# Optimization experiments

Measured on AMD Instinct MI355X. Metric: run time of the kernel, lower is better.

The kernel has to match this reference:

```python
import jax, jax.numpy as jnp
import numpy as np
from jax import lax

BATCH = 512
NUM_ITER = 5
NUM_CLASSES = 10
NUM_PRIMARY = 32 * 6 * 6  # 1152
CAPS_IN = 8
CAPS_OUT = 16
EPS = 1e-5


def _bn(x, g, b):
    # training-mode batchnorm over (N,H,W) per channel, NCHW
    m = x.mean(axis=(0, 2, 3), keepdims=True)
    v = x.var(axis=(0, 2, 3), keepdims=True)
    return g[None, :, None, None] * (x - m) * lax.rsqrt(v + EPS) + b[None, :, None, None]


def _conv(x, w, b, stride):
    y = lax.conv_general_dilated(x, w, (stride, stride), 'VALID',
                                 dimension_numbers=('NCHW', 'OIHW', 'NCHW'))
    return y + b[None, :, None, None]


def _squash(s):
    # per source: n / (n^2 + 1) * x
    n = jnp.linalg.norm(s, axis=-1, keepdims=True)
    return n / (n * n + 1.0) * s


def setup_inputs() -> dict:
    key = jax.random.key(0)
    ks = jax.random.split(key, 10)
    d = {
        'x': jax.random.normal(ks[0], (BATCH, 1, 28, 28), jnp.float32),
        'conv1_w': jax.random.normal(ks[1], (256, 1, 9, 9), jnp.float32) * 0.05,
        'conv1_b': jnp.zeros((256,), jnp.float32),
        'bn1_g': jnp.ones((256,), jnp.float32),
        'bn1_b': jnp.zeros((256,), jnp.float32),
        # 8 branch convs of (32,256,9,9) stacked into one (256,256,9,9) conv
        'conv2_w': jax.random.normal(ks[2], (256, 256, 9, 9), jnp.float32) * 0.01,
        'conv2_b': jnp.zeros((256,), jnp.float32),
        'bn2_g': jnp.ones((256,), jnp.float32),
        'bn2_b': jnp.zeros((256,), jnp.float32),
        'W': jax.random.normal(ks[3], (NUM_CLASSES, NUM_PRIMARY, CAPS_IN, CAPS_OUT), jnp.float32),
    }
    return d


def reference(x, conv1_w, conv1_b, bn1_g, bn1_b, conv2_w, conv2_b, bn2_g, bn2_b, W):
    B = x.shape[0]
    # input conv: (B,1,28,28) -> (B,256,20,20)
    y = jax.nn.relu(_bn(_conv(x, conv1_w, conv1_b, 1), bn1_g, bn1_b))
    # primary caps conv (8 branches fused): (B,256,6,6)
    z = jax.nn.relu(_bn(_conv(y, conv2_w, conv2_b, 2), bn2_g, bn2_b))
    # capsules: (B,8,32,6,6) -> (B, 1152, 8); capsule dim = branch index
    u = z.reshape(B, CAPS_IN, NUM_PRIMARY).transpose(0, 2, 1)
    # prediction vectors u_hat: (B, 10, 1152, 16)
    u_hat = jnp.einsum('bid,jide->bjie', u, W)

    def routing_step(b_log, _):
        c = jax.nn.softmax(b_log, axis=1)              # over 10 output caps
        s = jnp.einsum('bji,bjie->bje', c, u_hat)      # (B,10,16)
        v = _squash(s)
        b_log = b_log + jnp.einsum('bjie,bje->bji', u_hat, v)
        return b_log, v

    b0 = jnp.zeros((B, NUM_CLASSES, NUM_PRIMARY), u_hat.dtype)
    _, vs = lax.scan(routing_step, b0, None, length=NUM_ITER)
    return vs[-1]  # (B, 10, 16)
```

## Files before the change

### kernel.cpp

```cpp
#include <hip/hip_runtime.h>

typedef unsigned short u16;
typedef unsigned int   u32;
typedef __attribute__((ext_vector_type(8))) short bf16x8;
typedef __attribute__((ext_vector_type(4))) float f32x4;

__device__ __forceinline__ float bf2f(u16 u) { return __uint_as_float(((u32)u) << 16); }
__device__ __forceinline__ float bflo(u32 u) { return __uint_as_float(u << 16); }
__device__ __forceinline__ float bfhi(u32 u) { return __uint_as_float(u & 0xffff0000u); }
__device__ __forceinline__ u16 f2bf(float f) {
    u32 x = __float_as_uint(f);
    x += 0x7fffu + ((x >> 16) & 1u);
    return (u16)(x >> 16);
}
__device__ __forceinline__ u16 f2h(float f) {
    _Float16 h = (_Float16)f;
    return __builtin_bit_cast(u16, h);
}
__device__ __forceinline__ float h2f(u16 u) {
    return (float)__builtin_bit_cast(_Float16, u);
}

__global__ __launch_bounds__(256) void repack_w2_kernel(const float* __restrict__ w2,
                                                        u16* __restrict__ w2r) {
    int idx = blockIdx.x * 256 + threadIdx.x;
    int cil = idx & 31;
    int co  = (idx >> 5) & 255;
    int ccc = (idx >> 13) & 7;
    int kk  = idx >> 16;
    int ci  = ccc * 32 + cil;
    w2r[idx] = f2bf(w2[(size_t)co * 20736 + (size_t)ci * 81 + kk]);
}

__global__ __launch_bounds__(256) void repack_W_kernel(const float* __restrict__ W,
                                                       float* __restrict__ Wt2) {
    int idx = blockIdx.x * 256 + threadIdx.x;
    int d  = idx & 7;
    int je = (idx >> 3) % 160;
    int i  = idx / 1280;
    int j = je >> 4, e = je & 15;
    Wt2[idx] = W[(((size_t)j * 1152 + i) * 8 + d) * 16 + e];
}

__global__ __launch_bounds__(256) void conv1_kernel(const float* __restrict__ x,
                                                    const float* __restrict__ w1,
                                                    const float* __restrict__ b1,
                                                    u16* __restrict__ y,
                                                    float* __restrict__ sum1,
                                                    float* __restrict__ sumsq1) {
    __shared__ float xs[784];
    const int b = blockIdx.x;
    const int t = threadIdx.x;
    const float* xb = x + (size_t)b * 784;
    for (int idx = t; idx < 784; idx += 256) xs[idx] = xb[idx];
    float w[81];
#pragma unroll
    for (int q = 0; q < 81; ++q) w[q] = w1[(size_t)t * 81 + q];
    const float bias = b1[t];
    __syncthreads();

    float sl = 0.f, ssl = 0.f;
    u16* yb = y + (size_t)b * 400 * 256 + t;
    for (int oh = 0; oh < 20; ++oh) {
        float acc[20];
#pragma unroll
        for (int ow = 0; ow < 20; ++ow) acc[ow] = bias;
#pragma unroll
        for (int kh = 0; kh < 9; ++kh) {
            const float4* rp = (const float4*)(&xs[(oh + kh) * 28]);
            float r[28];
#pragma unroll
            for (int k4 = 0; k4 < 7; ++k4) {
                float4 f = rp[k4];
                r[k4 * 4 + 0] = f.x; r[k4 * 4 + 1] = f.y;
                r[k4 * 4 + 2] = f.z; r[k4 * 4 + 3] = f.w;
            }
#pragma unroll
            for (int kw = 0; kw < 9; ++kw) {
                const float wv = w[kh * 9 + kw];
#pragma unroll
                for (int ow = 0; ow < 20; ++ow)
                    acc[ow] = fmaf(wv, r[ow + kw], acc[ow]);
            }
        }
#pragma unroll
        for (int ow = 0; ow < 20; ++ow) {
            u16 q = f2bf(acc[ow]);
            float rv = bf2f(q);
            sl += rv; ssl += rv * rv;
            yb[(size_t)(oh * 20 + ow) * 256] = q;
        }
    }
    atomicAdd(&sum1[t], sl);
    atomicAdd(&sumsq1[t], ssl);
}

__global__ void finalize_bn_kernel(const float* __restrict__ sum,
                                   const float* __restrict__ sumsq,
                                   const float* __restrict__ gam,
                                   const float* __restrict__ bet,
                                   float* __restrict__ scale,
                                   float* __restrict__ shift, float inv_n) {
    int c = threadIdx.x;
    float m = sum[c] * inv_n;
    float var = sumsq[c] * inv_n - m * m;
    float sc = gam[c] * rsqrtf(var + 1e-5f);
    scale[c] = sc;
    shift[c] = bet[c] - m * sc;
}

__global__ __launch_bounds__(256) void bnpack_kernel(u32* __restrict__ y32,
                                                     const float* __restrict__ scale1,
                                                     const float* __restrict__ shift1) {
    const int b = blockIdx.x;
    const int t = threadIdx.x;
    const int c2 = (t & 127) * 2;
    const float s0 = scale1[c2],     s1 = scale1[c2 + 1];
    const float h0 = shift1[c2],     h1 = shift1[c2 + 1];
    u32* base = y32 + (size_t)b * 51200;
    for (int q = 0; q < 200; ++q) {
        const int idx = t + q * 256;
        u32 v = base[idx];
        float a = fmaxf(0.f, fmaf(s0, bflo(v), h0));
        float c = fmaxf(0.f, fmaf(s1, bfhi(v), h1));
        base[idx] = (u32)f2bf(a) | ((u32)f2bf(c) << 16);
    }
}

__global__ __launch_bounds__(256, 2) void conv2_mfma_kernel(const u16* __restrict__ y,
                                                            const u16* __restrict__ w2r,
                                                            const float* __restrict__ b2,
                                                            float* __restrict__ z_raw,
                                                            float* __restrict__ sum2,
                                                            float* __restrict__ sumsq2) {
    __shared__ __align__(16) u16 stg[240 * 136];
    const int g  = blockIdx.x >> 1;
    const int cb = (blockIdx.x & 1) * 128;
    const int b0 = g * 2;
    const int t = threadIdx.x;
    const int wave = t >> 6, lane = t & 63;
    const int n16 = lane & 15, quad = lane >> 4;
    const int img = wave & 1, c64 = wave >> 1;

    f32x4 zero = {0.f, 0.f, 0.f, 0.f};
    f32x4 acc[4][3];
#pragma unroll
    for (int ct = 0; ct < 4; ++ct)
#pragma unroll
        for (int pt = 0; pt < 3; ++pt) acc[ct][pt] = zero;

    int brow[3];
#pragma unroll
    for (int pt = 0; pt < 3; ++pt) {
        int pos = pt * 16 + n16; if (pos > 35) pos = 35;
        const int oh = (pos * 43) >> 8;
        const int ow = pos - oh * 6;
        brow[pt] = (img * 6 + oh) * 20 + 2 * ow;
    }

    const int laneoff = (cb + c64 * 64 + n16) * 32 + quad * 8;

    bf16x8 abuf[3][4];
    bf16x8 bbuf[2][3];

    auto loadA = [&](bf16x8 (&dst)[4], const u16* basep, int ittv) {
        const u16* wa = basep + (ittv >> 2) * 65536 + (ittv & 3) * 8192;
#pragma unroll
        for (int ct = 0; ct < 4; ++ct)
            dst[ct] = *((const bf16x8*)(wa + ct * 512));
    };
    auto loadB = [&](bf16x8 (&dst)[3], int ittv) {
        const int kw = ittv >> 2, ccc = ittv & 3;
#pragma unroll
        for (int pt = 0; pt < 3; ++pt)
            dst[pt] = *((const bf16x8*)(stg + (brow[pt] + kw) * 136
                                        + ccc * 32 + quad * 8));
    };

    {
        const u16* w0 = w2r + laneoff;
        loadA(abuf[0], w0, 0);
        loadA(abuf[1], w0, 1);
        loadA(abuf[2], w0, 2);
    }

    for (int kh = 0; kh < 9; ++kh) {
        for (int cp = 0; cp < 2; ++cp) {
            __syncthreads();
#pragma unroll
            for (int q = 0; q < 15; ++q) {
                const int v = t + q * 256;
                const int rI = v >> 4, c16 = v & 15;
                const int i2 = (rI >= 120) ? 1 : 0;
                const int rr = rI - i2 * 120;
                const int oh = rr / 20;
                const int iw = rr - oh * 20;
                const int ip = (2 * oh + kh) * 20 + iw;
                const uint4 d = *((const uint4*)(y + ((size_t)(b0 + i2) * 400 + ip) * 256
                                                 + cp * 128 + c16 * 8));
                *((uint4*)(stg + rI * 136 + c16 * 8)) = d;
            }
            __syncthreads();

            const int khn = (cp == 1) ? kh + 1 : kh;
            const int cpn = cp ^ 1;
            const u16* wbase = w2r + (size_t)kh * 589824 + (size_t)cp * 32768 + laneoff;
            const u16* wnext = w2r + (size_t)khn * 589824 + (size_t)cpn * 32768 + laneoff;

            loadB(bbuf[0], 0);
            loadB(bbuf[1], 1);

#pragma unroll
            for (int itt = 0; itt < 36; ++itt) {
                const int a_i = itt % 3, b_i = itt % 2;
#pragma unroll
                for (int ct = 0; ct < 4; ++ct)
#pragma unroll
                    for (int pt = 0; pt < 3; ++pt)
                        acc[ct][pt] = __builtin_amdgcn_mfma_f32_16x16x32_bf16(
                            abuf[a_i][ct], bbuf[b_i][pt], acc[ct][pt], 0, 0, 0);
                if (itt < 33) loadA(abuf[a_i], wbase, itt + 3);
                else          loadA(abuf[a_i], wnext, itt + 3 - 36);
                if (itt < 34) loadB(bbuf[b_i], itt + 2);
            }
        }
    }

#pragma unroll
    for (int ct = 0; ct < 4; ++ct) {
#pragma unroll
        for (int r = 0; r < 4; ++r) {
            const int co = cb + c64 * 64 + ct * 16 + quad * 4 + r;
            const float bias = b2[co];
            float s = 0.f, ss = 0.f;
#pragma unroll
            for (int pt = 0; pt < 3; ++pt) {
                const int pos = pt * 16 + n16;
                if (pos < 36) {
                    float v = acc[ct][pt][r] + bias;
                    z_raw[((size_t)(b0 + img) * 256 + co) * 36 + pos] = v;
                    s += v; ss += v * v;
                }
            }
#pragma unroll
            for (int m = 1; m < 16; m <<= 1) {
                s  += __shfl_xor(s,  m, 64);
                ss += __shfl_xor(ss, m, 64);
            }
            if (n16 == 0) { atomicAdd(&sum2[co], s); atomicAdd(&sumsq2[co], ss); }
        }
    }
}

__global__ __launch_bounds__(256) void ubuild_kernel(const float* __restrict__ z_raw,
                                                     const float* __restrict__ scale2,
                                                     const float* __restrict__ shift2,
                                                     u16* __restrict__ ut16) {
    const int b = blockIdx.x;
    const int t = threadIdx.x;
    const int d = t >> 5, m = t & 31;
    const float sc = scale2[t], sh = shift2[t];
    const float* zp = z_raw + ((size_t)b * 256 + t) * 36;
    u32* up = (u32*)(ut16 + ((size_t)b * 8 + d) * 1152 + m * 36);
#pragma unroll
    for (int q = 0; q < 18; ++q) {
        float v0 = fmaxf(0.f, fmaf(sc, zp[2 * q],     sh));
        float v1 = fmaxf(0.f, fmaf(sc, zp[2 * q + 1], sh));
        up[q] = (u32)f2h(v0) | ((u32)f2h(v1) << 16);
    }
}

__global__ __launch_bounds__(256) void uhat_kernel(const u16* __restrict__ ut16,
                                                   const float* __restrict__ Wt2,
                                                   u16* __restrict__ u_hat,
                                                   float* __restrict__ s0g) {
    __shared__ float utl[8 * 8 * 144];
    const int bg = blockIdx.x >> 3;
    const int ic = blockIdx.x & 7;
    const int b0 = bg * 8, i0 = ic * 144;
    for (int v = threadIdx.x; v < 8 * 8 * 144; v += 256) {
        int ii = v % 144; int d = (v / 144) & 7; int bb = v / 1152;
        utl[v] = h2f(ut16[(size_t)(b0 + bb) * 9216 + d * 1152 + i0 + ii]);
    }
    __syncthreads();
    for (int q = 0; q < 90; ++q) {
        int o = q * 256 + threadIdx.x;
        int ii = o / 160, je = o - ii * 160;
        const float* wp = Wt2 + ((size_t)(i0 + ii) * 160 + je) * 8;
        float w[8];
#pragma unroll
        for (int d = 0; d < 8; ++d) w[d] = wp[d];
#pragma unroll
        for (int bb = 0; bb < 8; ++bb) {
            float acc = 0.f;
#pragma unroll
            for (int d = 0; d < 8; ++d) acc = fmaf(w[d], utl[bb * 1152 + d * 144 + ii], acc);
            u_hat[(size_t)(b0 + bb) * 184320 + (size_t)(i0 + ii) * 160 + je] = f2h(acc);
        }
    }
    __syncthreads();
#pragma unroll
    for (int p = 0; p < 5; ++p) {
        const int pair = p * 256 + threadIdx.x;
        const int bb = pair / 160, je = pair - (pair / 160) * 160;
        const u16* up = u_hat + (size_t)(b0 + bb) * 184320 + (size_t)i0 * 160 + je;
        float s = 0.f;
        for (int ii = 0; ii < 144; ++ii) s += h2f(up[(size_t)ii * 160]);
        atomicAdd(&s0g[(size_t)(b0 + bb) * 160 + je], s);
    }
}

__global__ __launch_bounds__(384) void routing_kernel(const u16* __restrict__ u_hat,
                                                      const float* __restrict__ s0g,
                                                      float* __restrict__ out) {
    __shared__ __align__(16) u16 uhs[2][96 * 168];
    __shared__ float cl[10 * 96];
    __shared__ float part[320];
    __shared__ float sv[160];
    __shared__ float bls[12 * 96 * 11];
    const int t = threadIdx.x;
    const int b = blockIdx.x;
    const u16* uh = u_hat + (size_t)b * 184320;
    const int hB = (t < 320) ? (t / 160) : 0;
    const int je = (t < 320) ? (t - hB * 160) : 0;
    const int jB = je >> 4;

    uint4 rg[5];
    {
        const u16* src = uh;
#pragma unroll
        for (int q = 0; q < 5; ++q) {
            int v = t + q * 384, r = v / 20, c16 = v - r * 20;
            rg[q] = *((const uint4*)(src + r * 160 + c16 * 8));
        }
    }
    for (int v = t; v < 12 * 96 * 11; v += 384) bls[v] = 0.f;
    if (t < 160) sv[t] = 0.1f * s0g[(size_t)b * 160 + t];
    __syncthreads();
    if (t < 10) {
        float n2 = 0.f;
#pragma unroll
        for (int e2 = 0; e2 < 16; ++e2) { float xx = sv[t * 16 + e2]; n2 += xx * xx; }
        float n = sqrtf(n2);
        float f = n / (n2 + 1.f);
#pragma unroll
        for (int e2 = 0; e2 < 16; ++e2) sv[t * 16 + e2] *= f;
    }
#pragma unroll
    for (int q = 0; q < 5; ++q) {
        int v = t + q * 384, r = v / 20, c16 = v - r * 20;
        *((uint4*)(&uhs[0][r * 168 + c16 * 8])) = rg[q];
    }

    for (int k = 1; k <= 4; ++k) {
        float sacc = 0.f;
        for (int c = 0; c < 12; ++c) {
            const int p = c & 1;
            const bool last = (k == 4) && (c == 11);
            __syncthreads();
            if (!last) {
                const int nc = (c == 11) ? 0 : c + 1;
                const u16* src = uh + (size_t)nc * 15360;
#pragma unroll
                for (int q = 0; q < 5; ++q) {
                    int v = t + q * 384, r = v / 20, c16 = v - r * 20;
                    rg[q] = *((const uint4*)(src + r * 160 + c16 * 8));
                }
            }
            if (t < 96) {
                const u16* row = uhs[p] + t * 168;
                float* blrow = &bls[(c * 96 + t) * 11];
                float bj[10];
#pragma unroll
                for (int j = 0; j < 10; ++j) {
                    uint4 a = *((const uint4*)(row + j * 16));
                    uint4 bq = *((const uint4*)(row + j * 16 + 8));
                    const float* vv = &sv[j * 16];
                    float dj = h2f((u16)(a.x & 0xffff)) * vv[0]  + h2f((u16)(a.x >> 16)) * vv[1]
                             + h2f((u16)(a.y & 0xffff)) * vv[2]  + h2f((u16)(a.y >> 16)) * vv[3]
                             + h2f((u16)(a.z & 0xffff)) * vv[4]  + h2f((u16)(a.z >> 16)) * vv[5]
                             + h2f((u16)(a.w & 0xffff)) * vv[6]  + h2f((u16)(a.w >> 16)) * vv[7]
                             + h2f((u16)(bq.x & 0xffff)) * vv[8]  + h2f((u16)(bq.x >> 16)) * vv[9]
                             + h2f((u16)(bq.y & 0xffff)) * vv[10] + h2f((u16)(bq.y >> 16)) * vv[11]
                             + h2f((u16)(bq.z & 0xffff)) * vv[12] + h2f((u16)(bq.z >> 16)) * vv[13]
                             + h2f((u16)(bq.w & 0xffff)) * vv[14] + h2f((u16)(bq.w >> 16)) * vv[15];
                    float nb = blrow[j] + dj;
                    blrow[j] = nb;
                    bj[j] = nb;
                }
                float mx = bj[0];
#pragma unroll
                for (int j = 1; j < 10; ++j) mx = fmaxf(mx, bj[j]);
                float s = 0.f;
#pragma unroll
                for (int j = 0; j < 10; ++j) { bj[j] = __expf(bj[j] - mx); s += bj[j]; }
                float inv = 1.f / s;
#pragma unroll
                for (int j = 0; j < 10; ++j) cl[j * 96 + t] = bj[j] * inv;
            }
            __syncthreads();
            if (t < 320) {
                const int r0 = hB * 48;
#pragma unroll 4
                for (int il = 0; il < 48; ++il) {
                    const int r = r0 + il;
                    sacc = fmaf(cl[jB * 96 + r], h2f(uhs[p][r * 168 + je]), sacc);
                }
            }
            if (!last) {
#pragma unroll
                for (int q = 0; q < 5; ++q) {
                    int v = t + q * 384, r = v / 20, c16 = v - r * 20;
                    *((uint4*)(&uhs[p ^ 1][r * 168 + c16 * 8])) = rg[q];
                }
            }
        }
        __syncthreads();
        if (t < 320) part[t] = sacc;
        __syncthreads();
        if (t < 160) sv[t] = part[t] + part[t + 160];
        __syncthreads();
        if (t < 10) {
            float n2 = 0.f;
#pragma unroll
            for (int e2 = 0; e2 < 16; ++e2) { float xx = sv[t * 16 + e2]; n2 += xx * xx; }
            float n = sqrtf(n2);
            float f = n / (n2 + 1.f);
#pragma unroll
            for (int e2 = 0; e2 < 16; ++e2) sv[t * 16 + e2] *= f;
        }
    }
    __syncthreads();
    if (t < 160) out[(size_t)b * 160 + t] = sv[t];
}

extern "C" void kernel_launch(void* const* d_in, const int* in_sizes, int n_in,
                              void* d_out, int out_size, void* d_ws, size_t ws_size,
                              hipStream_t stream) {
    const float* x   = (const float*)d_in[0];
    const float* w1  = (const float*)d_in[1];
    const float* b1  = (const float*)d_in[2];
    const float* g1  = (const float*)d_in[3];
    const float* be1 = (const float*)d_in[4];
    const float* w2  = (const float*)d_in[5];
    const float* b2  = (const float*)d_in[6];
    const float* g2  = (const float*)d_in[7];
    const float* be2 = (const float*)d_in[8];
    const float* W   = (const float*)d_in[9];
    float* out = (float*)d_out;

    const size_t OFF_UHAT = 8192;
    const size_t OFF_Y    = 8192;
    const size_t OFF_W2R  = 104865792ull;
    const size_t OFF_Z    = 126099456ull;
    const size_t OFF_UT   = 188751872ull;
    const size_t OFF_S0   = 198189056ull;
    const size_t OFF_WT   = 207626240ull;
    const size_t WS_NEED  = 213524480ull;
    if (ws_size < WS_NEED) return;

    char* ws = (char*)d_ws;
    float* sum1   = (float*)(ws + 0);
    float* sumsq1 = (float*)(ws + 1024);
    float* sum2   = (float*)(ws + 2048);
    float* sumsq2 = (float*)(ws + 3072);
    float* scale1 = (float*)(ws + 4096);
    float* shift1 = (float*)(ws + 5120);
    float* scale2 = (float*)(ws + 6144);
    float* shift2 = (float*)(ws + 7168);
    u16*   y     = (u16*)(ws + OFF_Y);
    u16*   w2r   = (u16*)(ws + OFF_W2R);
    float* z_raw = (float*)(ws + OFF_Z);
    u16*   ut16  = (u16*)(ws + OFF_UT);
    float* s0g   = (float*)(ws + OFF_S0);
    float* Wt2   = (float*)(ws + OFF_WT);
    u16*   u_hat = (u16*)(ws + OFF_UHAT);

    hipMemsetAsync(ws, 0, 4096, stream);
    hipMemsetAsync(ws + OFF_S0, 0, 327680, stream);

    hipLaunchKernelGGL(repack_w2_kernel, dim3(20736), dim3(256), 0, stream, w2, w2r);
    hipLaunchKernelGGL(repack_W_kernel,  dim3(5760),  dim3(256), 0, stream, W, Wt2);
    hipLaunchKernelGGL(conv1_kernel,     dim3(512),   dim3(256), 0, stream,
                       x, w1, b1, y, sum1, sumsq1);
    hipLaunchKernelGGL(finalize_bn_kernel, dim3(1), dim3(256), 0, stream,
                       sum1, sumsq1, g1, be1, scale1, shift1, 1.f / 204800.f);
    hipLaunchKernelGGL(bnpack_kernel,    dim3(512),   dim3(256), 0, stream,
                       (u32*)y, scale1, shift1);
    hipLaunchKernelGGL(conv2_mfma_kernel, dim3(512),  dim3(256), 0, stream,
                       y, w2r, b2, z_raw, sum2, sumsq2);
    hipLaunchKernelGGL(finalize_bn_kernel, dim3(1), dim3(256), 0, stream,
                       sum2, sumsq2, g2, be2, scale2, shift2, 1.f / 18432.f);
    hipLaunchKernelGGL(ubuild_kernel,    dim3(512),   dim3(256), 0, stream,
                       z_raw, scale2, shift2, ut16);
    hipLaunchKernelGGL(uhat_kernel,      dim3(512),   dim3(256), 0, stream,
                       ut16, Wt2, u_hat, s0g);
    hipLaunchKernelGGL(routing_kernel,   dim3(512),   dim3(384), 0, stream,
                       u_hat, s0g, out);
}
```

Before: 1.041 ms.

## Double-buffer conv2 input staging with async global-to-LDS DMA and XOR swizzle

Replaces the synchronous register-mediated copy of input rows into shared memory with global_load_lds direct DMA into two ping-pong LDS buffers. Each stage is now a 64-channel slice instead of a 128-channel slice, so the next stage's load overlaps the MFMA work on the current one, and one barrier per stage replaces the previous two. The row-padded layout becomes an XOR-swizzled 64-wide layout to avoid LDS bank conflicts. The cost is twice as many stages and barriers, and correctness depends on when the async LDS writes become visible relative to the barrier.

```diff
diff --git a/kernel.cpp b/kernel.cpp
--- a/kernel.cpp
+++ b/kernel.cpp
@@ -133,7 +133,7 @@
                                                             float* __restrict__ z_raw,
                                                             float* __restrict__ sum2,
                                                             float* __restrict__ sumsq2) {
-    __shared__ __align__(16) u16 stg[240 * 136];
+    __shared__ __align__(16) u16 stg2[2][240 * 64];
     const int g  = blockIdx.x >> 1;
     const int cb = (blockIdx.x & 1) * 128;
     const int b0 = g * 2;
@@ -160,70 +160,88 @@
 
     const int laneoff = (cb + c64 * 64 + n16) * 32 + quad * 8;
 
+    u32 goff[8];
+#pragma unroll
+    for (int q = 0; q < 8; ++q) {
+        const int v = t + q * 256;
+        const int row = v >> 3, s = v & 7;
+        const int i2 = (row >= 120) ? 1 : 0;
+        const int rr = row - i2 * 120;
+        const int oh = rr / 20;
+        const int iw = rr - oh * 20;
+        goff[q] = (u32)(((b0 + i2) * 400 + 40 * oh + iw) * 256 + ((s ^ (row & 7)) << 3));
+    }
+
+    auto stage_dma = [&](int st_, u16* buf) {
+        const int kh_ = st_ >> 2, q4 = st_ & 3;
+        const int soff = kh_ * 5120 + q4 * 64;
+#pragma unroll
+        for (int q = 0; q < 8; ++q) {
+            if (q < 7 || t < 128) {
+                const int v = t + q * 256;
+                __builtin_amdgcn_global_load_lds(
+                    (const __attribute__((address_space(1))) void*)(y + goff[q] + soff),
+                    (__attribute__((address_space(3))) void*)(buf + (size_t)v * 8),
+                    16, 0, 0);
+            }
+        }
+    };
+
     bf16x8 abuf[3][4];
     bf16x8 bbuf[2][3];
 
     auto loadA = [&](bf16x8 (&dst)[4], const u16* basep, int ittv) {
-        const u16* wa = basep + (ittv >> 2) * 65536 + (ittv & 3) * 8192;
+        const u16* wa = basep + (ittv >> 1) * 65536 + (ittv & 1) * 8192;
 #pragma unroll
         for (int ct = 0; ct < 4; ++ct)
             dst[ct] = *((const bf16x8*)(wa + ct * 512));
     };
-    auto loadB = [&](bf16x8 (&dst)[3], int ittv) {
-        const int kw = ittv >> 2, ccc = ittv & 3;
-#pragma unroll
-        for (int pt = 0; pt < 3; ++pt)
-            dst[pt] = *((const bf16x8*)(stg + (brow[pt] + kw) * 136
-                                        + ccc * 32 + quad * 8));
+    auto loadB = [&](bf16x8 (&dst)[3], const u16* bufc, int ittv) {
+        const int kw = ittv >> 1;
+        const int cB = (ittv & 1) * 4 + quad;
+#pragma unroll
+        for (int pt = 0; pt < 3; ++pt) {
+            const int row = brow[pt] + kw;
+            dst[pt] = *((const bf16x8*)(bufc + row * 64 + ((cB ^ (row & 7)) << 3)));
+        }
     };
 
+    stage_dma(0, &stg2[0][0]);
     {
         const u16* w0 = w2r + laneoff;
         loadA(abuf[0], w0, 0);
         loadA(abuf[1], w0, 1);
         loadA(abuf[2], w0, 2);
     }
-
-    for (int kh = 0; kh < 9; ++kh) {
-        for (int cp = 0; cp < 2; ++cp) {
-            __syncthreads();
-#pragma unroll
-            for (int q = 0; q < 15; ++q) {
-                const int v = t + q * 256;
-                const int rI = v >> 4, c16 = v & 15;
-                const int i2 = (rI >= 120) ? 1 : 0;
-                const int rr = rI - i2 * 120;
-                const int oh = rr / 20;
-                const int iw = rr - oh * 20;
-                const int ip = (2 * oh + kh) * 20 + iw;
-                const uint4 d = *((const uint4*)(y + ((size_t)(b0 + i2) * 400 + ip) * 256
-                                                 + cp * 128 + c16 * 8));
-                *((uint4*)(stg + rI * 136 + c16 * 8)) = d;
-            }
-            __syncthreads();
-
-            const int khn = (cp == 1) ? kh + 1 : kh;
-            const int cpn = cp ^ 1;
-            const u16* wbase = w2r + (size_t)kh * 589824 + (size_t)cp * 32768 + laneoff;
-            const u16* wnext = w2r + (size_t)khn * 589824 + (size_t)cpn * 32768 + laneoff;
-
-            loadB(bbuf[0], 0);
-            loadB(bbuf[1], 1);
-
-#pragma unroll
-            for (int itt = 0; itt < 36; ++itt) {
-                const int a_i = itt % 3, b_i = itt % 2;
-#pragma unroll
-                for (int ct = 0; ct < 4; ++ct)
-#pragma unroll
-                    for (int pt = 0; pt < 3; ++pt)
-                        acc[ct][pt] = __builtin_amdgcn_mfma_f32_16x16x32_bf16(
-                            abuf[a_i][ct], bbuf[b_i][pt], acc[ct][pt], 0, 0, 0);
-                if (itt < 33) loadA(abuf[a_i], wbase, itt + 3);
-                else          loadA(abuf[a_i], wnext, itt + 3 - 36);
-                if (itt < 34) loadB(bbuf[b_i], itt + 2);
-            }
-        }
+    __syncthreads();
+
+    for (int st = 0; st < 36; ++st) {
+        u16* bufc = &stg2[st & 1][0];
+        if (st < 35) stage_dma(st + 1, &stg2[(st + 1) & 1][0]);
+
+        const int kh = st >> 2, q4 = st & 3;
+        const u16* wbase = w2r + (size_t)kh * 589824 + (size_t)q4 * 16384 + laneoff;
+        const int stn = (st < 35) ? st + 1 : st;
+        const u16* wnext = w2r + (size_t)(stn >> 2) * 589824
+                         + (size_t)(stn & 3) * 16384 + laneoff;
+
+        loadB(bbuf[0], bufc, 0);
+        loadB(bbuf[1], bufc, 1);
+
+#pragma unroll
+        for (int itt = 0; itt < 18; ++itt) {
+            const int a_i = itt % 3, b_i = itt % 2;
+#pragma unroll
+            for (int ct = 0; ct < 4; ++ct)
+#pragma unroll
+                for (int pt = 0; pt < 3; ++pt)
+                    acc[ct][pt] = __builtin_amdgcn_mfma_f32_16x16x32_bf16(
+                        abuf[a_i][ct], bbuf[b_i][pt], acc[ct][pt], 0, 0, 0);
+            if (itt < 15) loadA(abuf[a_i], wbase, itt + 3);
+            else          loadA(abuf[a_i], wnext, itt + 3 - 18);
+            if (itt < 16) loadB(bbuf[b_i], bufc, itt + 2);
+        }
+        __syncthreads();
     }
 
 #pragma unroll
```

Result: slower. 1.079 ms (+3.6%).

## Split conv2 over input-channel halves with 4-image blocks and merge partials

Applied to the files above, without the earlier changes.

The conv2 MFMA kernel now uses 512-thread blocks covering 4 images and 128 output channels, and splits the 256 input channels into two halves handled by separate blocks. Each half writes partial sums to its own buffer. A new zmerge kernel adds the partials with the bias and accumulates the BN statistics. The aim is to reuse weights across more images per block and to raise occupancy with a smaller shared staging buffer. The cost is an extra partial-sum buffer write and read plus one more kernel launch.

```diff
diff --git a/kernel.cpp b/kernel.cpp
--- a/kernel.cpp
+++ b/kernel.cpp
@@ -127,20 +127,20 @@
     }
 }
 
-__global__ __launch_bounds__(256, 2) void conv2_mfma_kernel(const u16* __restrict__ y,
+__global__ __launch_bounds__(512, 4) void conv2_mfma_kernel(const u16* __restrict__ y,
                                                             const u16* __restrict__ w2r,
-                                                            const float* __restrict__ b2,
-                                                            float* __restrict__ z_raw,
-                                                            float* __restrict__ sum2,
-                                                            float* __restrict__ sumsq2) {
-    __shared__ __align__(16) u16 stg[240 * 136];
-    const int g  = blockIdx.x >> 1;
-    const int cb = (blockIdx.x & 1) * 128;
-    const int b0 = g * 2;
+                                                            float* __restrict__ zp) {
+    __shared__ __align__(16) u16 stg[480 * 68];
+    const int h = blockIdx.x;
+    const int combo = (h & 7) >> 1;
+    const int cb  = combo >> 1;
+    const int cih = combo & 1;
+    const int gq  = ((h >> 3) << 1) + (h & 1);
+    const int b0  = gq * 4;
     const int t = threadIdx.x;
     const int wave = t >> 6, lane = t & 63;
     const int n16 = lane & 15, quad = lane >> 4;
-    const int img = wave & 1, c64 = wave >> 1;
+    const int img = wave & 3, c64 = wave >> 2;
 
     f32x4 zero = {0.f, 0.f, 0.f, 0.f};
     f32x4 acc[4][3];
@@ -158,98 +158,114 @@
         brow[pt] = (img * 6 + oh) * 20 + 2 * ow;
     }
 
-    const int laneoff = (cb + c64 * 64 + n16) * 32 + quad * 8;
+    const int laneoff = (cb * 128 + c64 * 64 + n16) * 32 + quad * 8;
 
     bf16x8 abuf[3][4];
     bf16x8 bbuf[2][3];
 
     auto loadA = [&](bf16x8 (&dst)[4], const u16* basep, int ittv) {
-        const u16* wa = basep + (ittv >> 2) * 65536 + (ittv & 3) * 8192;
+        const u16* wa = basep + (ittv >> 1) * 65536 + (ittv & 1) * 8192;
 #pragma unroll
         for (int ct = 0; ct < 4; ++ct)
             dst[ct] = *((const bf16x8*)(wa + ct * 512));
     };
     auto loadB = [&](bf16x8 (&dst)[3], int ittv) {
-        const int kw = ittv >> 2, ccc = ittv & 3;
+        const int kw = ittv >> 1;
+        const int cB = (ittv & 1) * 4 + quad;
 #pragma unroll
         for (int pt = 0; pt < 3; ++pt)
-            dst[pt] = *((const bf16x8*)(stg + (brow[pt] + kw) * 136
-                                        + ccc * 32 + quad * 8));
+            dst[pt] = *((const bf16x8*)(stg + (brow[pt] + kw) * 68 + cB * 8));
     };
 
     {
-        const u16* w0 = w2r + laneoff;
+        const u16* w0 = w2r + (size_t)(cih * 4) * 8192 + laneoff;
         loadA(abuf[0], w0, 0);
         loadA(abuf[1], w0, 1);
         loadA(abuf[2], w0, 2);
     }
 
-    for (int kh = 0; kh < 9; ++kh) {
-        for (int cp = 0; cp < 2; ++cp) {
-            __syncthreads();
-#pragma unroll
-            for (int q = 0; q < 15; ++q) {
-                const int v = t + q * 256;
-                const int rI = v >> 4, c16 = v & 15;
-                const int i2 = (rI >= 120) ? 1 : 0;
-                const int rr = rI - i2 * 120;
+    for (int st = 0; st < 18; ++st) {
+        const int kh = st >> 1, cp = st & 1;
+        __syncthreads();
+#pragma unroll
+        for (int q = 0; q < 8; ++q) {
+            if (q < 7 || t < 256) {
+                const int v = t + q * 512;
+                const int row = v >> 3, c8 = v & 7;
+                const int i4 = row / 120;
+                const int rr = row - i4 * 120;
                 const int oh = rr / 20;
                 const int iw = rr - oh * 20;
                 const int ip = (2 * oh + kh) * 20 + iw;
-                const uint4 d = *((const uint4*)(y + ((size_t)(b0 + i2) * 400 + ip) * 256
-                                                 + cp * 128 + c16 * 8));
-                *((uint4*)(stg + rI * 136 + c16 * 8)) = d;
-            }
-            __syncthreads();
-
-            const int khn = (cp == 1) ? kh + 1 : kh;
-            const int cpn = cp ^ 1;
-            const u16* wbase = w2r + (size_t)kh * 589824 + (size_t)cp * 32768 + laneoff;
-            const u16* wnext = w2r + (size_t)khn * 589824 + (size_t)cpn * 32768 + laneoff;
-
-            loadB(bbuf[0], 0);
-            loadB(bbuf[1], 1);
-
-#pragma unroll
-            for (int itt = 0; itt < 36; ++itt) {
-                const int a_i = itt % 3, b_i = itt % 2;
-#pragma unroll
-                for (int ct = 0; ct < 4; ++ct)
-#pragma unroll
-                    for (int pt = 0; pt < 3; ++pt)
-                        acc[ct][pt] = __builtin_amdgcn_mfma_f32_16x16x32_bf16(
-                            abuf[a_i][ct], bbuf[b_i][pt], acc[ct][pt], 0, 0, 0);
-                if (itt < 33) loadA(abuf[a_i], wbase, itt + 3);
-                else          loadA(abuf[a_i], wnext, itt + 3 - 36);
-                if (itt < 34) loadB(bbuf[b_i], itt + 2);
-            }
-        }
-    }
-
+                const uint4 d = *((const uint4*)(y + ((size_t)(b0 + i4) * 400 + ip) * 256
+                                                 + cih * 128 + cp * 64 + c8 * 8));
+                *((uint4*)(stg + row * 68 + c8 * 8)) = d;
+            }
+        }
+        __syncthreads();
+
+        const int stn = (st < 17) ? st + 1 : st;
+        const int khn = stn >> 1, cpn = stn & 1;
+        const u16* wbase = w2r + (size_t)kh * 589824
+                         + (size_t)(cih * 4 + cp * 2) * 8192 + laneoff;
+        const u16* wnext = w2r + (size_t)khn * 589824
+                         + (size_t)(cih * 4 + cpn * 2) * 8192 + laneoff;
+
+        loadB(bbuf[0], 0);
+        loadB(bbuf[1], 1);
+
+#pragma unroll
+        for (int itt = 0; itt < 18; ++itt) {
+            const int a_i = itt % 3, b_i = itt % 2;
+#pragma unroll
+            for (int ct = 0; ct < 4; ++ct)
+#pragma unroll
+                for (int pt = 0; pt < 3; ++pt)
+                    acc[ct][pt] = __builtin_amdgcn_mfma_f32_16x16x32_bf16(
+                        abuf[a_i][ct], bbuf[b_i][pt], acc[ct][pt], 0, 0, 0);
+            if (itt < 15) loadA(abuf[a_i], wbase, itt + 3);
+            else          loadA(abuf[a_i], wnext, itt + 3 - 18);
+            if (itt < 16) loadB(bbuf[b_i], itt + 2);
+        }
+    }
+
+    float* zb = zp + (size_t)cih * 4718592;
 #pragma unroll
     for (int ct = 0; ct < 4; ++ct) {
 #pragma unroll
         for (int r = 0; r < 4; ++r) {
-            const int co = cb + c64 * 64 + ct * 16 + quad * 4 + r;
-            const float bias = b2[co];
-            float s = 0.f, ss = 0.f;
+            const int co = cb * 128 + c64 * 64 + ct * 16 + quad * 4 + r;
 #pragma unroll
             for (int pt = 0; pt < 3; ++pt) {
                 const int pos = pt * 16 + n16;
-                if (pos < 36) {
-                    float v = acc[ct][pt][r] + bias;
-                    z_raw[((size_t)(b0 + img) * 256 + co) * 36 + pos] = v;
-                    s += v; ss += v * v;
-                }
-            }
-#pragma unroll
-            for (int m = 1; m < 16; m <<= 1) {
-                s  += __shfl_xor(s,  m, 64);
-                ss += __shfl_xor(ss, m, 64);
-            }
-            if (n16 == 0) { atomicAdd(&sum2[co], s); atomicAdd(&sumsq2[co], ss); }
-        }
-    }
+                if (pos < 36)
+                    zb[((size_t)(b0 + img) * 256 + co) * 36 + pos] = acc[ct][pt][r];
+            }
+        }
+    }
+}
+
+__global__ __launch_bounds__(256) void zmerge_kernel(float* __restrict__ z0,
+                                                     const float* __restrict__ z1,
+                                                     const float* __restrict__ b2,
+                                                     float* __restrict__ sum2,
+                                                     float* __restrict__ sumsq2) {
+    const int b = blockIdx.x, c = threadIdx.x;
+    const float bias = b2[c];
+    float4* p0 = (float4*)(z0 + ((size_t)b * 256 + c) * 36);
+    const float4* p1 = (const float4*)(z1 + ((size_t)b * 256 + c) * 36);
+    float s = 0.f, ss = 0.f;
+#pragma unroll
+    for (int q = 0; q < 9; ++q) {
+        float4 a = p0[q];
+        float4 d = p1[q];
+        a.x += d.x + bias; a.y += d.y + bias; a.z += d.z + bias; a.w += d.w + bias;
+        s  += a.x + a.y + a.z + a.w;
+        ss += a.x * a.x + a.y * a.y + a.z * a.z + a.w * a.w;
+        p0[q] = a;
+    }
+    atomicAdd(&sum2[c], s);
+    atomicAdd(&sumsq2[c], ss);
 }
 
 __global__ __launch_bounds__(256) void ubuild_kernel(const float* __restrict__ z_raw,
@@ -471,6 +487,7 @@
     u16*   y     = (u16*)(ws + OFF_Y);
     u16*   w2r   = (u16*)(ws + OFF_W2R);
     float* z_raw = (float*)(ws + OFF_Z);
+    float* z1    = (float*)(ws + OFF_Z + 18874368ull);
     u16*   ut16  = (u16*)(ws + OFF_UT);
     float* s0g   = (float*)(ws + OFF_S0);
     float* Wt2   = (float*)(ws + OFF_WT);
@@ -487,8 +504,10 @@
                        sum1, sumsq1, g1, be1, scale1, shift1, 1.f / 204800.f);
     hipLaunchKernelGGL(bnpack_kernel,    dim3(512),   dim3(256), 0, stream,
                        (u32*)y, scale1, shift1);
-    hipLaunchKernelGGL(conv2_mfma_kernel, dim3(512),  dim3(256), 0, stream,
-                       y, w2r, b2, z_raw, sum2, sumsq2);
+    hipLaunchKernelGGL(conv2_mfma_kernel, dim3(512),  dim3(512), 0, stream,
+                       y, w2r, z_raw);
+    hipLaunchKernelGGL(zmerge_kernel,    dim3(512),   dim3(256), 0, stream,
+                       z_raw, z1, b2, sum2, sumsq2);
     hipLaunchKernelGGL(finalize_bn_kernel, dim3(1), dim3(256), 0, stream,
                        sum2, sumsq2, g2, be2, scale2, shift2, 1.f / 18432.f);
     hipLaunchKernelGGL(ubuild_kernel,    dim3(512),   dim3(256), 0, stream,
```

Result: slower. 1.172 ms (+12.6%).
